# Optimization experiments

Hardware: AMD Instinct MI355X
Metric: run time of the kernel (lower is better)

## Reference

```python
import jax, jax.numpy as jnp
import numpy as np

DN = ('NCH', 'OIH', 'NCH')

def conv1d(x, w, b, pad):
    y = jax.lax.conv_general_dilated(x, w, (1,), [(pad, pad)], dimension_numbers=DN)
    return y if b is None else y + b[None, :, None]

def bn_eval(x, g, b, m, v, eps):
    s = g * jax.lax.rsqrt(v + eps)
    return x * s[None, :, None] + (b - m * s)[None, :, None]

def swish(x):
    return x * jax.nn.sigmoid(x)

def setup_inputs() -> dict:
    key = jax.random.key(0)
    ks = jax.random.split(key, 8)
    B, T, P = 16, 8192, 32
    inp = {
        'x': jax.random.normal(ks[0], (B, 1, T), jnp.float32),
        'conv_w': jax.random.normal(ks[1], (512, 1, 9), jnp.float32) * 0.1,
        'bn_g': jnp.ones((512,), jnp.float32),
        'bn_b': jnp.zeros((512,), jnp.float32),
        'bn_m': jnp.zeros((512,), jnp.float32),
        'bn_v': jnp.ones((512,), jnp.float32),
        'p1_w': jax.random.normal(ks[2], (P, 2, 31), jnp.float32) * 0.1,
        'p1_b': jnp.zeros((P,), jnp.float32),
        'pbn1_g': jnp.ones((P,), jnp.float32),
        'pbn1_b': jnp.zeros((P,), jnp.float32),
        'pbn1_m': jnp.zeros((P,), jnp.float32),
        'pbn1_v': jnp.ones((P,), jnp.float32),
        'p2_w': jax.random.normal(ks[3], (P, P, 15), jnp.float32) * 0.05,
        'p2_b': jnp.zeros((P,), jnp.float32),
        'pbn2_g': jnp.ones((P,), jnp.float32),
        'pbn2_b': jnp.zeros((P,), jnp.float32),
        'pbn2_m': jnp.zeros((P,), jnp.float32),
        'pbn2_v': jnp.ones((P,), jnp.float32),
        'p3_w': jax.random.normal(ks[4], (2, P, 15), jnp.float32) * 0.001,  # source scales last conv weight by 0.01
        'p3_b': jnp.full((2,), -np.log(2.0), jnp.float32),                 # source sets bias to -log(2)
        'norm_mean': jnp.ones((1,), jnp.float32),                           # eval-mode renorm buffer
    }
    return inp

def reference(x, conv_w, bn_g, bn_b, bn_m, bn_v,
              p1_w, p1_b, pbn1_g, pbn1_b, pbn1_m, pbn1_v,
              p2_w, p2_b, pbn2_g, pbn2_b, pbn2_m, pbn2_v,
              p3_w, p3_b, norm_mean):
    B, _, T = x.shape
    # main conv -> BN(eps=1e-3) -> GLU(dim=1); dropout is identity in eval
    h = conv1d(x, conv_w, None, 9 // 2)                 # [B, 512, T]
    h = bn_eval(h, bn_g, bn_b, bn_m, bn_v, 1e-3)
    a, g = jnp.split(h, 2, axis=1)
    features = a * jax.nn.sigmoid(g)                    # [B, 256, T]
    # predictor on cat([x, x*x])
    j = conv1d(jnp.concatenate([x, x * x], axis=1), p1_w, p1_b, 15)
    j = swish(bn_eval(j, pbn1_g, pbn1_b, pbn1_m, pbn1_v, 1e-5))
    j = conv1d(j, p2_w, p2_b, 7)
    j = swish(bn_eval(j, pbn2_g, pbn2_b, pbn2_m, pbn2_v, 1e-5))
    j = conv1d(j, p3_w, p3_b, 7)                        # [B, 2, T]
    weights = jax.nn.sigmoid(j[:, 0, :])                # [B, T]
    moves = jax.nn.sigmoid(j[:, 1, :])
    bmoves = moves
    moves = moves * norm_mean[0]                        # eval: renorm = norm_mean buffer
    # CIF-style dynamic pooling (row_pool), vectorized over batch
    feats = jnp.transpose(features, (0, 2, 1))          # [B, T, C]
    fw = feats * weights[..., None]
    poses = jnp.cumsum(jax.lax.stop_gradient(moves), axis=1)  # moves.detach() in source
    floors = jnp.floor(poses)
    w1 = 1.0 - (poses - floors)
    w2 = poses - floors
    fl = floors.astype(jnp.int32)
    ce = fl + 1
    Lmax = T + 2  # static bound: poses <= T so ceil index <= T+1
    C = fw.shape[2]
    def pool(fw_i, fl_i, ce_i, w1_i, w2_i):
        out = jnp.zeros((Lmax, C), fw_i.dtype)
        out = out.at[fl_i].add(w1_i[:, None] * fw_i)
        out = out.at[ce_i].add(w2_i[:, None] * fw_i)
        return out
    x_evs = jax.vmap(pool)(fw, fl, ce, w1, w2)          # [B, Lmax, C]
    lens = fl[:, -1] + 2                                 # int(ceils[-1]) + 1
    x_evs = jnp.transpose(x_evs, (0, 2, 1))             # [B, C, Lmax]
    pad = 3 - (Lmax % 3)
    x_evs = jnp.pad(x_evs, ((0, 0), (0, 0), (0, pad)))
    return x_evs, lens, bmoves, weights
```

## Files before the change

kernel.cpp:

```cpp
#include <hip/hip_runtime.h>
#include <math.h>

static constexpr int TT = 8192;
static constexpr int LFULL = 8196;
static constexpr int BSTRIDE = LFULL + 2;

static constexpr size_t XE_OFF   = 0;
static constexpr size_t LENS_OFF = (size_t)16*256*LFULL;
static constexpr size_t BM_OFF   = LENS_OFF + 16;
static constexpr size_t WT_OFF   = BM_OFF + (size_t)16*TT;

static constexpr size_t U_OFF     = 0;
static constexpr size_t V_OFF     = U_OFF + (size_t)16*32*TT;
static constexpr size_t MOVES_OFF = V_OFF + (size_t)16*32*TT;
static constexpr size_t C1_OFF    = MOVES_OFF + (size_t)16*TT;
static constexpr size_t C2_OFF    = C1_OFF + (size_t)16*TT;
static constexpr size_t BND_OFF   = U_OFF;

__device__ __forceinline__ float sig_(float z) { return 1.0f / (1.0f + __expf(-z)); }

typedef float f4v __attribute__((ext_vector_type(4)));
__device__ __forceinline__ void nt_store4(float* p, float a, float b, float c, float d) {
    f4v v = {a, b, c, d};
    __builtin_nontemporal_store(v, (f4v*)p);
}

__global__ __launch_bounds__(256) void k_conv12(
    const float* __restrict__ x,
    const float* __restrict__ p1w, const float* __restrict__ p1b,
    const float* __restrict__ g1, const float* __restrict__ b1,
    const float* __restrict__ m1, const float* __restrict__ v1,
    const float* __restrict__ p2w, const float* __restrict__ p2b,
    const float* __restrict__ g2, const float* __restrict__ b2,
    const float* __restrict__ m2, const float* __restrict__ v2,
    float* __restrict__ vout)
{
    __shared__ float xin[320];
    __shared__ float w1t[2 * 992];
    __shared__ float uld[32 * 276];
    __shared__ float w2t[32 * 256];
    const int tid = threadIdx.x;
    const int b = blockIdx.y;
    const int t0 = blockIdx.x * 256;
    const int ch = blockIdx.z;

    for (int idx = tid; idx < 320; idx += 256) {
        int id = t0 - 22 + idx;
        xin[idx] = (id >= 0 && id < TT) ? x[b * TT + id] : 0.f;
    }
    for (int idx = tid; idx < 1984; idx += 256) {
        int c = idx / 62; int r = idx - c * 62; int ci = r / 31; int k = r - ci * 31;
        w1t[ci * 992 + c * 31 + k] = p1w[idx];
    }
    for (int idx = tid; idx < 32 * 256; idx += 256) {
        int ci = idx >> 8; int r = idx & 255; int cl2 = r >> 4; int k = r & 15;
        w2t[idx] = (k < 15) ? p2w[(ch * 16 + cl2) * 480 + ci * 15 + k] : 0.f;
    }
    __syncthreads();

    {
        const int cB = tid & 31, pg = tid >> 5;
        const float s1v = g1[cB] * rsqrtf(v1[cB] + 1e-5f);
        const float sh1 = b1[cB] - m1[cB] * s1v;
        const float bias1 = p1b[cB];
        const int base = pg * 36;
        const float* wA = &w1t[cB * 31];
        const float* wB = &w1t[992 + cB * 31];
#pragma unroll
        for (int h = 0; h < 5; ++h) {
            const int off = h * 8;
            const int len = (h < 4) ? 8 : 4;
            const int nld = (h < 4) ? 10 : 9;
            float win[40], wsq[40];
            const float4* xp = (const float4*)(&xin[base + off]);
            for (int r = 0; r < nld; ++r) {
                float4 q = xp[r];
                win[4*r] = q.x; win[4*r+1] = q.y; win[4*r+2] = q.z; win[4*r+3] = q.w;
            }
            for (int i = 0; i < 4 * nld; ++i) wsq[i] = win[i] * win[i];
            float acc[8];
#pragma unroll
            for (int i = 0; i < 8; ++i) acc[i] = bias1;
#pragma unroll
            for (int k = 0; k < 31; ++k) {
                const float a = wA[k], bw = wB[k];
                for (int i = 0; i < len; ++i) {
                    acc[i] = fmaf(a, win[i + k], acc[i]);
                    acc[i] = fmaf(bw, wsq[i + k], acc[i]);
                }
            }
            for (int i = 0; i < len; ++i) {
                const int tl = base + off + i;
                if (tl < 270) {
                    const float z = fmaf(acc[i], s1v, sh1);
                    uld[cB * 276 + tl] = z * sig_(z);
                }
            }
        }
    }
    __syncthreads();

    const int tg = tid >> 4, cl = tid & 15;
    const int c2 = ch * 16 + cl;
    float acc2[16];
    const float bias2 = p2b[c2];
#pragma unroll
    for (int i = 0; i < 16; ++i) acc2[i] = bias2;

    for (int ci = 0; ci < 32; ++ci) {
        float win[32];
        const float4* wp = (const float4*)(&uld[ci * 276 + tg * 16]);
#pragma unroll
        for (int r = 0; r < 8; ++r) {
            float4 q = wp[r];
            win[4*r] = q.x; win[4*r+1] = q.y; win[4*r+2] = q.z; win[4*r+3] = q.w;
        }
        float w[16];
        const float4* wqp = (const float4*)(&w2t[ci * 256 + cl * 16]);
#pragma unroll
        for (int r = 0; r < 4; ++r) {
            float4 q = wqp[r];
            w[4*r] = q.x; w[4*r+1] = q.y; w[4*r+2] = q.z; w[4*r+3] = q.w;
        }
#pragma unroll
        for (int k = 0; k < 15; ++k) {
#pragma unroll
            for (int i = 0; i < 16; ++i) acc2[i] = fmaf(w[k], win[i + k], acc2[i]);
        }
    }
    const float s = g2[c2] * rsqrtf(v2[c2] + 1e-5f);
    const float sh = b2[c2] - m2[c2] * s;
    float o[16];
#pragma unroll
    for (int i = 0; i < 16; ++i) { float z = fmaf(acc2[i], s, sh); o[i] = z * sig_(z); }
    float* vp = &vout[((size_t)(b * 32 + c2)) * TT + t0 + tg * 16];
#pragma unroll
    for (int r = 0; r < 4; ++r)
        ((float4*)vp)[r] = make_float4(o[4*r], o[4*r+1], o[4*r+2], o[4*r+3]);
}

__global__ __launch_bounds__(256) void k_conv3(
    const float* __restrict__ vin,
    const float* __restrict__ p3w, const float* __restrict__ p3b,
    const float* __restrict__ nm,
    float* __restrict__ outw, float* __restrict__ outbm, float* __restrict__ moves)
{
    __shared__ float vld[32 * 276];
    __shared__ float wsh[960];
    const int tid = threadIdx.x;
    const int b = blockIdx.y;
    const int t0 = blockIdx.x * 256;

    for (int idx = tid; idx < 32 * 272; idx += 256) {
        int ci = idx / 272, tl = idx - ci * 272;
        int tg = t0 - 7 + tl;
        float val = 0.f;
        if (tl < 270 && tg >= 0 && tg < TT) val = vin[((size_t)(b * 32 + ci)) * TT + tg];
        vld[ci * 276 + tl] = val;
    }
    for (int idx = tid; idx < 960; idx += 256) wsh[idx] = p3w[idx];
    __syncthreads();

    const int g = tid >> 2;
    const int q = tid & 3;
    float acc[8];
#pragma unroll
    for (int i = 0; i < 8; ++i) acc[i] = 0.f;

#pragma unroll
    for (int i = 0; i < 8; ++i) {
        const int ci = q + 4 * i;
        float win[20];
        const float4* wp = (const float4*)(&vld[ci * 276 + g * 4]);
#pragma unroll
        for (int r = 0; r < 5; ++r) {
            float4 v4 = wp[r];
            win[4*r] = v4.x; win[4*r+1] = v4.y; win[4*r+2] = v4.z; win[4*r+3] = v4.w;
        }
        const float* w0 = &wsh[ci * 15];
        const float* w1 = &wsh[480 + ci * 15];
#pragma unroll
        for (int k = 0; k < 15; ++k) {
            const float a = w0[k], gw = w1[k];
#pragma unroll
            for (int tt = 0; tt < 4; ++tt) {
                acc[tt]     = fmaf(a,  win[k + tt], acc[tt]);
                acc[4 + tt] = fmaf(gw, win[k + tt], acc[4 + tt]);
            }
        }
    }
#pragma unroll
    for (int i = 0; i < 8; ++i) {
        acc[i] += __shfl_xor(acc[i], 1, 64);
        acc[i] += __shfl_xor(acc[i], 2, 64);
    }
    if (q == 0) {
        const float nmv = nm[0];
        const float b0 = p3b[0], b1 = p3b[1];
        const int t = t0 + g * 4;
        float4 wv = make_float4(sig_(acc[0]+b0), sig_(acc[1]+b0), sig_(acc[2]+b0), sig_(acc[3]+b0));
        float4 bm = make_float4(sig_(acc[4]+b1), sig_(acc[5]+b1), sig_(acc[6]+b1), sig_(acc[7]+b1));
        float4 mv = make_float4(bm.x*nmv, bm.y*nmv, bm.z*nmv, bm.w*nmv);
        *(float4*)&outw[b * TT + t]  = wv;
        *(float4*)&outbm[b * TT + t] = bm;
        *(float4*)&moves[b * TT + t] = mv;
    }
}

__global__ __launch_bounds__(1024) void k_scan(
    const float* __restrict__ moves, const float* __restrict__ wts,
    float* __restrict__ coef1, float* __restrict__ coef2,
    int* __restrict__ bnd, float* __restrict__ lens)
{
    __shared__ float wsum[16];
    const int tid = threadIdx.x;
    const int b = blockIdx.x;
    const int lane = tid & 63, wv = tid >> 6;
    float carry = 0.f;

    int* bb = &bnd[b * BSTRIDE];
    for (int i = tid; i < BSTRIDE; i += 1024) bb[i] = TT;
    if (tid == 0) { bb[0] = 0; bb[1] = 0; }
    __syncthreads();

    const float4* mv4 = (const float4*)&moves[b * TT];
    const float4* wt4 = (const float4*)&wts[b * TT];
    float4* c14 = (float4*)&coef1[b * TT];
    float4* c24 = (float4*)&coef2[b * TT];

    for (int chunk = 0; chunk < 2; ++chunk) {
        const int idx = chunk * 1024 + tid;
        float4 m = mv4[idx];
        const float s = m.x + m.y + m.z + m.w;
        float v = s;
#pragma unroll
        for (int off = 1; off < 64; off <<= 1) {
            float n = __shfl_up(v, off, 64);
            if (lane >= off) v += n;
        }
        if (lane == 63) wsum[wv] = v;
        __syncthreads();
        float pre = carry;
        for (int w = 0; w < wv; ++w) pre += wsum[w];
        float tot = 0.f;
#pragma unroll
        for (int w = 0; w < 16; ++w) tot += wsum[w];
        const float base = pre + (v - s);
        const float p0 = base + m.x;
        const float p1 = p0 + m.y;
        const float p2 = p1 + m.z;
        const float p3 = p2 + m.w;
        const float4 w4 = wt4[idx];
        const float fr0 = p0 - floorf(p0), fr1 = p1 - floorf(p1);
        const float fr2 = p2 - floorf(p2), fr3 = p3 - floorf(p3);
        c14[idx] = make_float4((1.f - fr0) * w4.x, (1.f - fr1) * w4.y,
                               (1.f - fr2) * w4.z, (1.f - fr3) * w4.w);
        c24[idx] = make_float4(fr0 * w4.x, fr1 * w4.y, fr2 * w4.z, fr3 * w4.w);
        {
            int lf = (int)floorf(base) + 1;
            const int lfe = (int)floorf(p3);
            const int tbase = idx << 2;
            for (; lf <= lfe; ++lf) {
                const float lff = (float)lf;
                int t = tbase;
                if (p0 >= lff) { }
                else if (p1 >= lff) t += 1;
                else if (p2 >= lff) t += 2;
                else t += 3;
                if (lf + 1 < BSTRIDE) bb[lf + 1] = t;
            }
        }
        if (chunk == 1 && tid == 1023) lens[b] = floorf(p3) + 2.0f;
        carry += tot;
        __syncthreads();
    }
}

static constexpr int LTILE = 32;
static constexpr int CHK = 256;
static constexpr int NPOOLX = (LFULL + LTILE - 1) / LTILE;

__global__ __launch_bounds__(256) void k_pool(
    const float* __restrict__ x,
    const float* __restrict__ cw,
    const float* __restrict__ bng, const float* __restrict__ bnb,
    const float* __restrict__ bnm, const float* __restrict__ bnv,
    const float* __restrict__ coef1, const float* __restrict__ coef2,
    const int* __restrict__ bnd, const float* __restrict__ lens,
    float* __restrict__ xevs)
{
    __shared__ float out_lds[256 * 33];
    __shared__ float4 xl4[68];
    __shared__ float4 c1l4[CHK / 4], c2l4[CHK / 4];
    __shared__ int lbs[LTILE + 2];
    float* xl = (float*)xl4;
    float* c1l = (float*)c1l4;
    float* c2l = (float*)c2l4;

    const int tid = threadIdx.x;
    const int b = blockIdx.y;

    if (blockIdx.x >= NPOOLX) {
        const int zx = blockIdx.x - NPOOLX;
        const int zs = (((int)lens[b]) + 15) & ~15;
        if (zs >= LFULL) return;
        const int n4 = (LFULL - zs) >> 2;
        for (int r = 0; r < 4; ++r) {
            float* row = &xevs[((size_t)(b * 256 + zx * 4 + r)) * LFULL + zs];
            for (int i = tid; i < n4; i += 256) nt_store4(row + 4 * i, 0.f, 0.f, 0.f, 0.f);
        }
        return;
    }

    const int l0 = blockIdx.x * LTILE;
    const int LTa = min(LTILE, LFULL - l0);

    if (tid < LTa + 2) lbs[tid] = bnd[b * BSTRIDE + l0 + tid];
    __syncthreads();

    const int t_lo = lbs[0];
    const int t_hi = lbs[LTa + 1];
    if (t_lo >= t_hi) return;

    const size_t rowbase = (size_t)b * 256 * LFULL + l0;

#pragma unroll
    for (int li = 0; li < 33; ++li) out_lds[tid * 33 + li] = 0.f;

    const int c = tid;
    float wa[9], wg[9];
#pragma unroll
    for (int k = 0; k < 9; ++k) { wa[k] = cw[c * 9 + k]; wg[k] = cw[(c + 256) * 9 + k]; }
    const float sa = bng[c] * rsqrtf(bnv[c] + 1e-3f);
    const float sha = bnb[c] - bnm[c] * sa;
    const float sg = bng[c + 256] * rsqrtf(bnv[c + 256] + 1e-3f);
    const float shg = bnb[c + 256] - bnm[c + 256] * sg;

    const float* xg = &x[b * TT];
    const float* c1g = &coef1[b * TT];
    const float* c2g = &coef2[b * TT];

    float accA = 0.f, accB = 0.f;
    int j = 0;
    int nb = lbs[1];

    for (int cs = t_lo; cs < t_hi; cs += CHK) {
        const int ce = min(cs + CHK, t_hi);
        const int len = ce - cs;
        __syncthreads();
        for (int idx = tid; idx < len + 12; idx += 256) {
            int id = cs - 4 + idx;
            xl[idx] = (id >= 0 && id < TT) ? xg[id] : 0.f;
        }
        if (tid < len) { c1l[tid] = c1g[cs + tid]; c2l[tid] = c2g[cs + tid]; }
        __syncthreads();

        const int len4 = len >> 2;
        for (int g = 0; g < len4; ++g) {
            float4 A = xl4[g], Bq = xl4[g + 1], Cq = xl4[g + 2];
            float w[12] = {A.x, A.y, A.z, A.w, Bq.x, Bq.y, Bq.z, Bq.w, Cq.x, Cq.y, Cq.z, Cq.w};
            float f[4];
#pragma unroll
            for (int i = 0; i < 4; ++i) {
                float s0 = 0.f, s1 = 0.f;
#pragma unroll
                for (int k = 0; k < 9; ++k) { s0 = fmaf(wa[k], w[i + k], s0); s1 = fmaf(wg[k], w[i + k], s1); }
                const float av = fmaf(s0, sa, sha);
                const float gv = fmaf(s1, sg, shg);
                f[i] = av * sig_(gv);
            }
            float4 c1v = c1l4[g], c2v = c2l4[g];
            const float c1a[4] = {c1v.x, c1v.y, c1v.z, c1v.w};
            const float c2a[4] = {c2v.x, c2v.y, c2v.z, c2v.w};
            const int tb = cs + (g << 2);
#pragma unroll
            for (int i = 0; i < 4; ++i) {
                const int t = tb + i;
                while (t >= nb) {
                    int li = j - 1;
                    if (li >= 0 && li < LTa) out_lds[c * 33 + li] = accA;
                    accA = accB; accB = 0.f;
                    ++j;
                    nb = lbs[j + 1];
                }
                accA = fmaf(c1a[i], f[i], accA);
                accB = fmaf(c2a[i], f[i], accB);
            }
        }
        for (int t = cs + (len4 << 2); t < ce; ++t) {
            const int il = t - cs;
            float s0 = 0.f, s1 = 0.f;
#pragma unroll
            for (int k = 0; k < 9; ++k) { float xv = xl[il + k]; s0 = fmaf(wa[k], xv, s0); s1 = fmaf(wg[k], xv, s1); }
            const float av = fmaf(s0, sa, sha);
            const float gv = fmaf(s1, sg, shg);
            const float f0 = av * sig_(gv);
            while (t >= nb) {
                int li = j - 1;
                if (li >= 0 && li < LTa) out_lds[c * 33 + li] = accA;
                accA = accB; accB = 0.f;
                ++j;
                nb = lbs[j + 1];
            }
            accA = fmaf(c1l[il], f0, accA);
            accB = fmaf(c2l[il], f0, accB);
        }
    }
    {
        int li = j - 1;
        if (li >= 0 && li < LTa) out_lds[c * 33 + li] = accA;
    }
    __syncthreads();

#pragma unroll
    for (int it = 0; it < 8; ++it) {
        int idx4 = it * 256 + tid;
        int cc = idx4 >> 3, q = (idx4 & 7) << 2;
        if (q < LTa) {
            nt_store4(&xevs[rowbase + (size_t)cc * LFULL + q],
                      out_lds[cc * 33 + q + 0], out_lds[cc * 33 + q + 1],
                      out_lds[cc * 33 + q + 2], out_lds[cc * 33 + q + 3]);
        }
    }
}

extern "C" void kernel_launch(void* const* d_in, const int* in_sizes, int n_in,
                              void* d_out, int out_size, void* d_ws, size_t ws_size,
                              hipStream_t stream) {
    (void)in_sizes; (void)n_in; (void)out_size; (void)ws_size;
    const float* x      = (const float*)d_in[0];
    const float* conv_w = (const float*)d_in[1];
    const float* bn_g   = (const float*)d_in[2];
    const float* bn_b   = (const float*)d_in[3];
    const float* bn_m   = (const float*)d_in[4];
    const float* bn_v   = (const float*)d_in[5];
    const float* p1_w   = (const float*)d_in[6];
    const float* p1_b   = (const float*)d_in[7];
    const float* pbn1_g = (const float*)d_in[8];
    const float* pbn1_b = (const float*)d_in[9];
    const float* pbn1_m = (const float*)d_in[10];
    const float* pbn1_v = (const float*)d_in[11];
    const float* p2_w   = (const float*)d_in[12];
    const float* p2_b   = (const float*)d_in[13];
    const float* pbn2_g = (const float*)d_in[14];
    const float* pbn2_b = (const float*)d_in[15];
    const float* pbn2_m = (const float*)d_in[16];
    const float* pbn2_v = (const float*)d_in[17];
    const float* p3_w   = (const float*)d_in[18];
    const float* p3_b   = (const float*)d_in[19];
    const float* nm     = (const float*)d_in[20];

    float* out = (float*)d_out;
    float* ws  = (float*)d_ws;
    float* v     = ws + V_OFF;
    float* moves = ws + MOVES_OFF;
    float* coef1 = ws + C1_OFF;
    float* coef2 = ws + C2_OFF;
    int*   bnd   = (int*)(ws + BND_OFF);
    float* xevs  = out + XE_OFF;
    float* lens  = out + LENS_OFF;
    float* bmv   = out + BM_OFF;
    float* wts   = out + WT_OFF;

    k_conv12<<<dim3(32, 16, 2), 256, 0, stream>>>(
        x, p1_w, p1_b, pbn1_g, pbn1_b, pbn1_m, pbn1_v,
        p2_w, p2_b, pbn2_g, pbn2_b, pbn2_m, pbn2_v, v);
    k_conv3<<<dim3(32, 16), 256, 0, stream>>>(v, p3_w, p3_b, nm, wts, bmv, moves);
    k_scan<<<16, 1024, 0, stream>>>(moves, wts, coef1, coef2, bnd, lens);
    k_pool<<<dim3(NPOOLX + 64, 16), 256, 0, stream>>>(
        x, conv_w, bn_g, bn_b, bn_m, bn_v, coef1, coef2, bnd, lens, xevs);
}
```

Measured before the change: 338.2 us.

## Fuse conv1/conv2/conv3 predictor stages into one kernel with halo recompute

Merges the conv12 and conv3 kernels into a single kernel. Each block now computes all 32 conv2 channels, plus extra halo columns, and keeps the result in shared memory so conv3 runs without the global round trip through the v buffer. The conv2 weight tile in shared memory is XOR-swizzled to avoid bank conflicts, and launch bounds now request 2 blocks per CU. In exchange the grid shrinks from 1024 to 512 blocks, each block does redundant halo work and more serial steps, and occupancy or parallelism may drop.

```diff
diff --git a/kernel.cpp b/kernel.cpp
--- a/kernel.cpp
+++ b/kernel.cpp
@@ -25,7 +25,9 @@
     __builtin_nontemporal_store(v, (f4v*)p);
 }
 
-__global__ __launch_bounds__(256) void k_conv12(
+static constexpr int US = 292;
+
+__global__ __launch_bounds__(256, 2) void k_convall(
     const float* __restrict__ x,
     const float* __restrict__ p1w, const float* __restrict__ p1b,
     const float* __restrict__ g1, const float* __restrict__ b1,
@@ -33,19 +35,20 @@
     const float* __restrict__ p2w, const float* __restrict__ p2b,
     const float* __restrict__ g2, const float* __restrict__ b2,
     const float* __restrict__ m2, const float* __restrict__ v2,
-    float* __restrict__ vout)
+    const float* __restrict__ p3w, const float* __restrict__ p3b,
+    const float* __restrict__ nm,
+    float* __restrict__ outw, float* __restrict__ outbm, float* __restrict__ moves)
 {
-    __shared__ float xin[320];
-    __shared__ float w1t[2 * 992];
-    __shared__ float uld[32 * 276];
-    __shared__ float w2t[32 * 256];
+    __shared__ __align__(16) float xin[320];
+    __shared__ __align__(16) float w1t[2 * 992];
+    __shared__ __align__(16) float uld[32 * US + 4];
+    __shared__ __align__(16) float w2t[32 * 256];
     const int tid = threadIdx.x;
     const int b = blockIdx.y;
     const int t0 = blockIdx.x * 256;
-    const int ch = blockIdx.z;
 
     for (int idx = tid; idx < 320; idx += 256) {
-        int id = t0 - 22 + idx;
+        int id = t0 - 29 + idx;
         xin[idx] = (id >= 0 && id < TT) ? x[b * TT + id] : 0.f;
     }
     for (int idx = tid; idx < 1984; idx += 256) {
@@ -54,7 +57,9 @@
     }
     for (int idx = tid; idx < 32 * 256; idx += 256) {
         int ci = idx >> 8; int r = idx & 255; int cl2 = r >> 4; int k = r & 15;
-        w2t[idx] = (k < 15) ? p2w[(ch * 16 + cl2) * 480 + ci * 15 + k] : 0.f;
+        int sw = (cl2 >> 1) & 3;
+        int phys = ci * 256 + cl2 * 16 + ((((k >> 2) ^ sw) << 2) | (k & 3));
+        w2t[phys] = (k < 15) ? p2w[cl2 * 480 + ci * 15 + k] : 0.f;
     }
     __syncthreads();
 
@@ -89,11 +94,19 @@
                     acc[i] = fmaf(bw, wsq[i + k], acc[i]);
                 }
             }
-            for (int i = 0; i < len; ++i) {
-                const int tl = base + off + i;
-                if (tl < 270) {
-                    const float z = fmaf(acc[i], s1v, sh1);
-                    uld[cB * 276 + tl] = z * sig_(z);
+#pragma unroll
+            for (int qq = 0; qq < 8; qq += 4) {
+                if (qq < len) {
+                    const int ul0 = base + off + qq;
+                    if (ul0 < 284) {
+                        f4v o;
+#pragma unroll
+                        for (int i = 0; i < 4; ++i) {
+                            const float z = fmaf(acc[qq + i], s1v, sh1);
+                            o[i] = z * sig_(z);
+                        }
+                        *(f4v*)&uld[cB * US + ul0] = o;
+                    }
                 }
             }
         }
@@ -101,109 +114,256 @@
     __syncthreads();
 
     const int tg = tid >> 4, cl = tid & 15;
-    const int c2 = ch * 16 + cl;
-    float acc2[16];
-    const float bias2 = p2b[c2];
-#pragma unroll
-    for (int i = 0; i < 16; ++i) acc2[i] = bias2;
-
-    for (int ci = 0; ci < 32; ++ci) {
-        float win[32];
-        const float4* wp = (const float4*)(&uld[ci * 276 + tg * 16]);
-#pragma unroll
-        for (int r = 0; r < 8; ++r) {
-            float4 q = wp[r];
-            win[4*r] = q.x; win[4*r+1] = q.y; win[4*r+2] = q.z; win[4*r+3] = q.w;
-        }
-        float w[16];
-        const float4* wqp = (const float4*)(&w2t[ci * 256 + cl * 16]);
+    const int swz = ((cl >> 1) & 3) << 2;
+    const int wv = tid >> 6;
+    const int lam = tid & 63;
+    const int clT = lam & 15;
+    const int sub = lam >> 4;
+    const int swzT = ((clT >> 1) & 3) << 2;
+    const int vl0T = 256 + 4 * wv;
+
+    float vres0[16], vres1[16];
+    float vt0[4], vt1[4];
+
+    {
+        const int c2 = cl;
+        float acc2[16];
+        const float bias2 = p2b[c2];
+#pragma unroll
+        for (int i = 0; i < 16; ++i) acc2[i] = bias2;
+        for (int ci = 0; ci < 32; ++ci) {
+            float win[32];
+            const float4* wp = (const float4*)(&uld[ci * US + tg * 16]);
+#pragma unroll
+            for (int r = 0; r < 8; ++r) {
+                float4 q = wp[r];
+                win[4*r] = q.x; win[4*r+1] = q.y; win[4*r+2] = q.z; win[4*r+3] = q.w;
+            }
+            float w[16];
+            const float* wrow = &w2t[ci * 256 + cl * 16];
+#pragma unroll
+            for (int r = 0; r < 4; ++r) {
+                float4 q = *(const float4*)(&wrow[(4 * r) ^ swz]);
+                w[4*r] = q.x; w[4*r+1] = q.y; w[4*r+2] = q.z; w[4*r+3] = q.w;
+            }
+#pragma unroll
+            for (int k = 0; k < 15; ++k)
+#pragma unroll
+                for (int i = 0; i < 16; ++i) acc2[i] = fmaf(w[k], win[i + k], acc2[i]);
+        }
+        const float s = g2[c2] * rsqrtf(v2[c2] + 1e-5f);
+        const float sh = b2[c2] - m2[c2] * s;
+        const int tvb = t0 - 7 + tg * 16;
+#pragma unroll
+        for (int i = 0; i < 16; ++i) {
+            const float z = fmaf(acc2[i], s, sh);
+            const float vvv = z * sig_(z);
+            const int tv = tvb + i;
+            vres0[i] = (tv >= 0 && tv < TT) ? vvv : 0.f;
+        }
+        {
+            const int c2T = clT;
+            float acc4[4] = {0.f, 0.f, 0.f, 0.f};
+#pragma unroll
+            for (int j = 0; j < 8; ++j) {
+                const int ci = sub + 4 * j;
+                float win[20];
+                const float4* wp = (const float4*)(&uld[ci * US + vl0T]);
+#pragma unroll
+                for (int r = 0; r < 5; ++r) {
+                    float4 q = wp[r];
+                    win[4*r] = q.x; win[4*r+1] = q.y; win[4*r+2] = q.z; win[4*r+3] = q.w;
+                }
+                float w[16];
+                const float* wrow = &w2t[ci * 256 + clT * 16];
+#pragma unroll
+                for (int r = 0; r < 4; ++r) {
+                    float4 q = *(const float4*)(&wrow[(4 * r) ^ swzT]);
+                    w[4*r] = q.x; w[4*r+1] = q.y; w[4*r+2] = q.z; w[4*r+3] = q.w;
+                }
+#pragma unroll
+                for (int k = 0; k < 15; ++k)
+#pragma unroll
+                    for (int i = 0; i < 4; ++i) acc4[i] = fmaf(w[k], win[i + k], acc4[i]);
+            }
+#pragma unroll
+            for (int i = 0; i < 4; ++i) {
+                acc4[i] += __shfl_xor(acc4[i], 16, 64);
+                acc4[i] += __shfl_xor(acc4[i], 32, 64);
+            }
+            const float sT = g2[c2T] * rsqrtf(v2[c2T] + 1e-5f);
+            const float shT = b2[c2T] - m2[c2T] * sT;
+            const float bT = p2b[c2T];
+#pragma unroll
+            for (int i = 0; i < 4; ++i) {
+                const float z = fmaf(acc4[i] + bT, sT, shT);
+                const float vvv = z * sig_(z);
+                const int tv = t0 - 7 + vl0T + i;
+                vt0[i] = (tv >= 0 && tv < TT) ? vvv : 0.f;
+            }
+        }
+    }
+    __syncthreads();
+
+    for (int idx = tid; idx < 32 * 256; idx += 256) {
+        int ci = idx >> 8; int r = idx & 255; int cl2 = r >> 4; int k = r & 15;
+        int sw = (cl2 >> 1) & 3;
+        int phys = ci * 256 + cl2 * 16 + ((((k >> 2) ^ sw) << 2) | (k & 3));
+        w2t[phys] = (k < 15) ? p2w[(16 + cl2) * 480 + ci * 15 + k] : 0.f;
+    }
+    {
+        float* wsh = w1t;
+        for (int idx = tid; idx < 960; idx += 256) wsh[idx] = p3w[idx];
+    }
+    __syncthreads();
+
+    {
+        const int c2 = 16 + cl;
+        float acc2[16];
+        const float bias2 = p2b[c2];
+#pragma unroll
+        for (int i = 0; i < 16; ++i) acc2[i] = bias2;
+        for (int ci = 0; ci < 32; ++ci) {
+            float win[32];
+            const float4* wp = (const float4*)(&uld[ci * US + tg * 16]);
+#pragma unroll
+            for (int r = 0; r < 8; ++r) {
+                float4 q = wp[r];
+                win[4*r] = q.x; win[4*r+1] = q.y; win[4*r+2] = q.z; win[4*r+3] = q.w;
+            }
+            float w[16];
+            const float* wrow = &w2t[ci * 256 + cl * 16];
+#pragma unroll
+            for (int r = 0; r < 4; ++r) {
+                float4 q = *(const float4*)(&wrow[(4 * r) ^ swz]);
+                w[4*r] = q.x; w[4*r+1] = q.y; w[4*r+2] = q.z; w[4*r+3] = q.w;
+            }
+#pragma unroll
+            for (int k = 0; k < 15; ++k)
+#pragma unroll
+                for (int i = 0; i < 16; ++i) acc2[i] = fmaf(w[k], win[i + k], acc2[i]);
+        }
+        const float s = g2[c2] * rsqrtf(v2[c2] + 1e-5f);
+        const float sh = b2[c2] - m2[c2] * s;
+        const int tvb = t0 - 7 + tg * 16;
+#pragma unroll
+        for (int i = 0; i < 16; ++i) {
+            const float z = fmaf(acc2[i], s, sh);
+            const float vvv = z * sig_(z);
+            const int tv = tvb + i;
+            vres1[i] = (tv >= 0 && tv < TT) ? vvv : 0.f;
+        }
+        {
+            const int c2T = 16 + clT;
+            float acc4[4] = {0.f, 0.f, 0.f, 0.f};
+#pragma unroll
+            for (int j = 0; j < 8; ++j) {
+                const int ci = sub + 4 * j;
+                float win[20];
+                const float4* wp = (const float4*)(&uld[ci * US + vl0T]);
+#pragma unroll
+                for (int r = 0; r < 5; ++r) {
+                    float4 q = wp[r];
+                    win[4*r] = q.x; win[4*r+1] = q.y; win[4*r+2] = q.z; win[4*r+3] = q.w;
+                }
+                float w[16];
+                const float* wrow = &w2t[ci * 256 + clT * 16];
+#pragma unroll
+                for (int r = 0; r < 4; ++r) {
+                    float4 q = *(const float4*)(&wrow[(4 * r) ^ swzT]);
+                    w[4*r] = q.x; w[4*r+1] = q.y; w[4*r+2] = q.z; w[4*r+3] = q.w;
+                }
+#pragma unroll
+                for (int k = 0; k < 15; ++k)
+#pragma unroll
+                    for (int i = 0; i < 4; ++i) acc4[i] = fmaf(w[k], win[i + k], acc4[i]);
+            }
+#pragma unroll
+            for (int i = 0; i < 4; ++i) {
+                acc4[i] += __shfl_xor(acc4[i], 16, 64);
+                acc4[i] += __shfl_xor(acc4[i], 32, 64);
+            }
+            const float sT = g2[c2T] * rsqrtf(v2[c2T] + 1e-5f);
+            const float shT = b2[c2T] - m2[c2T] * sT;
+            const float bT = p2b[c2T];
+#pragma unroll
+            for (int i = 0; i < 4; ++i) {
+                const float z = fmaf(acc4[i] + bT, sT, shT);
+                const float vvv = z * sig_(z);
+                const int tv = t0 - 7 + vl0T + i;
+                vt1[i] = (tv >= 0 && tv < TT) ? vvv : 0.f;
+            }
+        }
+    }
+    __syncthreads();
+
+    {
+        float* vbuf = uld;
 #pragma unroll
         for (int r = 0; r < 4; ++r) {
-            float4 q = wqp[r];
-            w[4*r] = q.x; w[4*r+1] = q.y; w[4*r+2] = q.z; w[4*r+3] = q.w;
-        }
-#pragma unroll
-        for (int k = 0; k < 15; ++k) {
-#pragma unroll
-            for (int i = 0; i < 16; ++i) acc2[i] = fmaf(w[k], win[i + k], acc2[i]);
-        }
-    }
-    const float s = g2[c2] * rsqrtf(v2[c2] + 1e-5f);
-    const float sh = b2[c2] - m2[c2] * s;
-    float o[16];
-#pragma unroll
-    for (int i = 0; i < 16; ++i) { float z = fmaf(acc2[i], s, sh); o[i] = z * sig_(z); }
-    float* vp = &vout[((size_t)(b * 32 + c2)) * TT + t0 + tg * 16];
-#pragma unroll
-    for (int r = 0; r < 4; ++r)
-        ((float4*)vp)[r] = make_float4(o[4*r], o[4*r+1], o[4*r+2], o[4*r+3]);
-}
-
-__global__ __launch_bounds__(256) void k_conv3(
-    const float* __restrict__ vin,
-    const float* __restrict__ p3w, const float* __restrict__ p3b,
-    const float* __restrict__ nm,
-    float* __restrict__ outw, float* __restrict__ outbm, float* __restrict__ moves)
-{
-    __shared__ float vld[32 * 276];
-    __shared__ float wsh[960];
-    const int tid = threadIdx.x;
-    const int b = blockIdx.y;
-    const int t0 = blockIdx.x * 256;
-
-    for (int idx = tid; idx < 32 * 272; idx += 256) {
-        int ci = idx / 272, tl = idx - ci * 272;
-        int tg = t0 - 7 + tl;
-        float val = 0.f;
-        if (tl < 270 && tg >= 0 && tg < TT) val = vin[((size_t)(b * 32 + ci)) * TT + tg];
-        vld[ci * 276 + tl] = val;
-    }
-    for (int idx = tid; idx < 960; idx += 256) wsh[idx] = p3w[idx];
-    __syncthreads();
-
-    const int g = tid >> 2;
-    const int q = tid & 3;
-    float acc[8];
-#pragma unroll
-    for (int i = 0; i < 8; ++i) acc[i] = 0.f;
-
-#pragma unroll
-    for (int i = 0; i < 8; ++i) {
-        const int ci = q + 4 * i;
-        float win[20];
-        const float4* wp = (const float4*)(&vld[ci * 276 + g * 4]);
-#pragma unroll
-        for (int r = 0; r < 5; ++r) {
-            float4 v4 = wp[r];
-            win[4*r] = v4.x; win[4*r+1] = v4.y; win[4*r+2] = v4.z; win[4*r+3] = v4.w;
-        }
-        const float* w0 = &wsh[ci * 15];
-        const float* w1 = &wsh[480 + ci * 15];
-#pragma unroll
-        for (int k = 0; k < 15; ++k) {
-            const float a = w0[k], gw = w1[k];
-#pragma unroll
-            for (int tt = 0; tt < 4; ++tt) {
-                acc[tt]     = fmaf(a,  win[k + tt], acc[tt]);
-                acc[4 + tt] = fmaf(gw, win[k + tt], acc[4 + tt]);
-            }
-        }
-    }
-#pragma unroll
-    for (int i = 0; i < 8; ++i) {
-        acc[i] += __shfl_xor(acc[i], 1, 64);
-        acc[i] += __shfl_xor(acc[i], 2, 64);
-    }
-    if (q == 0) {
-        const float nmv = nm[0];
-        const float b0 = p3b[0], b1 = p3b[1];
-        const int t = t0 + g * 4;
-        float4 wv = make_float4(sig_(acc[0]+b0), sig_(acc[1]+b0), sig_(acc[2]+b0), sig_(acc[3]+b0));
-        float4 bm = make_float4(sig_(acc[4]+b1), sig_(acc[5]+b1), sig_(acc[6]+b1), sig_(acc[7]+b1));
-        float4 mv = make_float4(bm.x*nmv, bm.y*nmv, bm.z*nmv, bm.w*nmv);
-        *(float4*)&outw[b * TT + t]  = wv;
-        *(float4*)&outbm[b * TT + t] = bm;
-        *(float4*)&moves[b * TT + t] = mv;
+            f4v a = {vres0[4*r], vres0[4*r+1], vres0[4*r+2], vres0[4*r+3]};
+            *(f4v*)&vbuf[cl * US + tg * 16 + 4 * r] = a;
+        }
+#pragma unroll
+        for (int r = 0; r < 4; ++r) {
+            f4v a = {vres1[4*r], vres1[4*r+1], vres1[4*r+2], vres1[4*r+3]};
+            *(f4v*)&vbuf[(16 + cl) * US + tg * 16 + 4 * r] = a;
+        }
+        if (sub == 0) {
+            f4v a = {vt0[0], vt0[1], vt0[2], vt0[3]};
+            *(f4v*)&vbuf[clT * US + vl0T] = a;
+            f4v c = {vt1[0], vt1[1], vt1[2], vt1[3]};
+            *(f4v*)&vbuf[(16 + clT) * US + vl0T] = c;
+        }
+    }
+    __syncthreads();
+
+    {
+        const float* vbuf = uld;
+        const float* wsh = w1t;
+        const int g = tid >> 2;
+        const int q3 = tid & 3;
+        float acc[8];
+#pragma unroll
+        for (int i = 0; i < 8; ++i) acc[i] = 0.f;
+#pragma unroll
+        for (int i = 0; i < 8; ++i) {
+            const int ci = q3 + 4 * i;
+            float win[20];
+            const float4* wp = (const float4*)(&vbuf[ci * US + g * 4]);
+#pragma unroll
+            for (int r = 0; r < 5; ++r) {
+                float4 v4 = wp[r];
+                win[4*r] = v4.x; win[4*r+1] = v4.y; win[4*r+2] = v4.z; win[4*r+3] = v4.w;
+            }
+            const float* w0 = &wsh[ci * 15];
+            const float* w1p = &wsh[480 + ci * 15];
+#pragma unroll
+            for (int k = 0; k < 15; ++k) {
+                const float a = w0[k], gw = w1p[k];
+#pragma unroll
+                for (int t4 = 0; t4 < 4; ++t4) {
+                    acc[t4]     = fmaf(a,  win[k + t4], acc[t4]);
+                    acc[4 + t4] = fmaf(gw, win[k + t4], acc[4 + t4]);
+                }
+            }
+        }
+#pragma unroll
+        for (int i = 0; i < 8; ++i) {
+            acc[i] += __shfl_xor(acc[i], 1, 64);
+            acc[i] += __shfl_xor(acc[i], 2, 64);
+        }
+        if (q3 == 0) {
+            const float nmv = nm[0];
+            const float b0 = p3b[0], b1v = p3b[1];
+            const int t = t0 + g * 4;
+            float4 wvv = make_float4(sig_(acc[0]+b0), sig_(acc[1]+b0), sig_(acc[2]+b0), sig_(acc[3]+b0));
+            float4 bm = make_float4(sig_(acc[4]+b1v), sig_(acc[5]+b1v), sig_(acc[6]+b1v), sig_(acc[7]+b1v));
+            float4 mv = make_float4(bm.x*nmv, bm.y*nmv, bm.z*nmv, bm.w*nmv);
+            *(float4*)&outw[b * TT + t]  = wvv;
+            *(float4*)&outbm[b * TT + t] = bm;
+            *(float4*)&moves[b * TT + t] = mv;
+        }
     }
 }
 
@@ -452,7 +612,6 @@
 
     float* out = (float*)d_out;
     float* ws  = (float*)d_ws;
-    float* v     = ws + V_OFF;
     float* moves = ws + MOVES_OFF;
     float* coef1 = ws + C1_OFF;
     float* coef2 = ws + C2_OFF;
@@ -462,10 +621,10 @@
     float* bmv   = out + BM_OFF;
     float* wts   = out + WT_OFF;
 
-    k_conv12<<<dim3(32, 16, 2), 256, 0, stream>>>(
+    k_convall<<<dim3(32, 16), 256, 0, stream>>>(
         x, p1_w, p1_b, pbn1_g, pbn1_b, pbn1_m, pbn1_v,
-        p2_w, p2_b, pbn2_g, pbn2_b, pbn2_m, pbn2_v, v);
-    k_conv3<<<dim3(32, 16), 256, 0, stream>>>(v, p3_w, p3_b, nm, wts, bmv, moves);
+        p2_w, p2_b, pbn2_g, pbn2_b, pbn2_m, pbn2_v,
+        p3_w, p3_b, nm, wts, bmv, moves);
     k_scan<<<16, 1024, 0, stream>>>(moves, wts, coef1, coef2, bnd, lens);
     k_pool<<<dim3(NPOOLX + 64, 16), 256, 0, stream>>>(
         x, conv_w, bn_g, bn_b, bn_m, bn_v, coef1, coef2, bnd, lens, xevs);
```

New measurement: 374.8 us. 1.11x slower.
